# Kernel optimization log

Measured on AMD Instinct MI355X. Metric: run time of the kernel, lower is better.

## Reference

```python
import jax, jax.numpy as jnp
import numpy as np

N_NODES = 50000
N_GRAPHS = 512
NEG_SLOPE = 0.2
EPS = 1e-16


def gat_conv(x, src, dst, W, a_src, a_dst, b):
    """PyG GATConv (heads=1, self-loops already appended, eval mode)."""
    h = x @ W                                   # [N, out]
    as_ = h @ a_src                             # [N]
    ad_ = h @ a_dst                             # [N]
    e = jax.nn.leaky_relu(as_[src] + ad_[dst], NEG_SLOPE)  # [E]
    # segment softmax over destination node
    m = jax.ops.segment_max(e, dst, num_segments=N_NODES)
    ee = jnp.exp(e - m[dst])
    s = jax.ops.segment_sum(ee, dst, num_segments=N_NODES)
    alpha = ee / (s[dst] + EPS)                 # [E]
    out = jax.ops.segment_sum(h[src] * alpha[:, None], dst, num_segments=N_NODES)
    return out + b


def setup_inputs() -> dict:
    key = jax.random.key(0)
    ks = jax.random.split(key, 16)
    vocab, d_model, hidden = 32000, 128, 128
    node_ids = jax.random.randint(ks[0], (N_NODES,), 0, vocab)
    edge_index = jax.random.randint(ks[1], (2, 800000), 0, N_NODES)
    batch = jnp.sort(jax.random.randint(ks[2], (N_NODES,), 0, N_GRAPHS))
    emb = jax.random.normal(ks[3], (vocab, d_model), jnp.float32) * 0.02

    def layer(k, din, dout):
        k1, k2, k3 = jax.random.split(k, 3)
        W = jax.random.normal(k1, (din, dout), jnp.float32) / np.sqrt(din)
        a_s = jax.random.normal(k2, (dout,), jnp.float32) / np.sqrt(dout)
        a_d = jax.random.normal(k3, (dout,), jnp.float32) / np.sqrt(dout)
        b = jnp.zeros((dout,), jnp.float32)
        return W, a_s, a_d, b

    W1, as1, ad1, b1 = layer(ks[4], d_model, hidden)
    W2, as2, ad2, b2 = layer(ks[5], hidden, hidden)
    W3, as3, ad3, b3 = layer(ks[6], hidden, hidden)
    return dict(node_ids=node_ids, edge_index=edge_index, batch=batch, emb=emb,
                W1=W1, as1=as1, ad1=ad1, b1=b1,
                W2=W2, as2=as2, ad2=ad2, b2=b2,
                W3=W3, as3=as3, ad3=ad3, b3=b3)


def reference(node_ids, edge_index, batch, emb,
              W1, as1, ad1, b1, W2, as2, ad2, b2, W3, as3, ad3, b3):
    # add self-loops (PyG GATConv default)
    loop = jnp.arange(N_NODES, dtype=edge_index.dtype)
    src = jnp.concatenate([edge_index[0], loop])
    dst = jnp.concatenate([edge_index[1], loop])

    x = emb[node_ids]                                   # [N, d_model]
    x = jax.nn.relu(gat_conv(x, src, dst, W1, as1, ad1, b1))
    x = jax.nn.relu(gat_conv(x, src, dst, W2, as2, ad2, b2))
    x = gat_conv(x, src, dst, W3, as3, ad3, b3)

    # global mean pool over graphs
    sums = jax.ops.segment_sum(x, batch, num_segments=N_GRAPHS)
    cnts = jax.ops.segment_sum(jnp.ones((N_NODES,), x.dtype), batch, num_segments=N_GRAPHS)
    return sums / jnp.maximum(cnts, 1.0)[:, None]       # [n_graphs, hidden]
```

## Files before the change

### kernel.cpp

```cpp
#include <hip/hip_runtime.h>
#include <hip/hip_fp16.h>
#include <math.h>

#define N_NODES    50000
#define N_EDGES_IN 800000
#define N_EDGES    850000
#define N_GRAPHS   512
#define NEG_SLOPE  0.2f
#define EPS_F      1e-16f

#define NB_COARSE  196
#define NSUB       8
#define NBINS      (NB_COARSE*NSUB)

typedef _Float16 half8 __attribute__((ext_vector_type(8)));
typedef float    f32x4 __attribute__((ext_vector_type(4)));

__global__ __launch_bounds__(256) void k_gemm(const void* __restrict__ xsrc,
                                              const int* __restrict__ ids,
                                              const float* __restrict__ W,
                                              const float* __restrict__ a_s,
                                              const float* __restrict__ a_d,
                                              _Float16* __restrict__ hH,
                                              float* __restrict__ as_,
                                              float* __restrict__ ad_) {
    __shared__ _Float16 WT[128][136];
    __shared__ _Float16 Xs[128][72];
    int t = threadIdx.x;
    int row0 = blockIdx.x * 128;
    int w = t >> 6, lane = t & 63;
    int n = lane & 15, quad = lane >> 4;

    #pragma unroll
    for (int i = 0; i < 16; i++) {
        int q = t + i * 256;
        int k = q >> 5;
        int n4 = (q & 31) * 4;
        float4 v = *(const float4*)(W + (size_t)k * 128 + n4);
        WT[n4 + 0][k] = (_Float16)v.x;
        WT[n4 + 1][k] = (_Float16)v.y;
        WT[n4 + 2][k] = (_Float16)v.z;
        WT[n4 + 3][k] = (_Float16)v.w;
    }

    f32x4 acc[2][8] = {};
    for (int kc = 0; kc < 2; kc++) {
        if (kc) __syncthreads();
        if (ids == nullptr) {
            const _Float16* xH = (const _Float16*)xsrc;
            #pragma unroll
            for (int i = 0; i < 4; i++) {
                int q = t + i * 256;
                int r = q >> 3, o8 = (q & 7) * 8;
                int gr = row0 + r; if (gr >= N_NODES) gr = N_NODES - 1;
                *(half8*)&Xs[r][o8] = *(const half8*)&xH[(size_t)gr * 128 + kc * 64 + o8];
            }
        } else {
            const float* xf = (const float*)xsrc;
            #pragma unroll
            for (int i = 0; i < 4; i++) {
                int q = t + i * 256;
                int r = q >> 3, o8 = (q & 7) * 8;
                int gr = row0 + r; if (gr >= N_NODES) gr = N_NODES - 1;
                const float* src = xf + (size_t)ids[gr] * 128 + kc * 64 + o8;
                float4 v0 = *(const float4*)src;
                float4 v1 = *(const float4*)(src + 4);
                half8 hv;
                hv[0] = (_Float16)v0.x; hv[1] = (_Float16)v0.y;
                hv[2] = (_Float16)v0.z; hv[3] = (_Float16)v0.w;
                hv[4] = (_Float16)v1.x; hv[5] = (_Float16)v1.y;
                hv[6] = (_Float16)v1.z; hv[7] = (_Float16)v1.w;
                *(half8*)&Xs[r][o8] = hv;
            }
        }
        __syncthreads();
        #pragma unroll
        for (int ks = 0; ks < 2; ks++) {
            int ko = ks * 32 + quad * 8;
            half8 a0 = *(const half8*)&Xs[w * 32 + n][ko];
            half8 a1 = *(const half8*)&Xs[w * 32 + 16 + n][ko];
            int kg = kc * 64 + ko;
            #pragma unroll
            for (int c = 0; c < 8; c++) {
                half8 b = *(const half8*)&WT[c * 16 + n][kg];
                acc[0][c] = __builtin_amdgcn_mfma_f32_16x16x32_f16(a0, b, acc[0][c], 0, 0, 0);
                acc[1][c] = __builtin_amdgcn_mfma_f32_16x16x32_f16(a1, b, acc[1][c], 0, 0, 0);
            }
        }
    }

    float sa[8], da[8];
    #pragma unroll
    for (int c = 0; c < 8; c++) { sa[c] = a_s[c * 16 + n]; da[c] = a_d[c * 16 + n]; }
    #pragma unroll
    for (int r = 0; r < 2; r++) {
        float ps[4] = {0.f, 0.f, 0.f, 0.f}, pd[4] = {0.f, 0.f, 0.f, 0.f};
        #pragma unroll
        for (int reg = 0; reg < 4; reg++) {
            int row = row0 + w * 32 + r * 16 + quad * 4 + reg;
            bool ok = row < N_NODES;
            #pragma unroll
            for (int c = 0; c < 8; c++) {
                float v = acc[r][c][reg];
                ps[reg] += v * sa[c];
                pd[reg] += v * da[c];
                if (ok) hH[(size_t)row * 128 + c * 16 + n] = (_Float16)v;
            }
        }
        #pragma unroll
        for (int off = 1; off < 16; off <<= 1) {
            #pragma unroll
            for (int reg = 0; reg < 4; reg++) {
                ps[reg] += __shfl_xor(ps[reg], off, 64);
                pd[reg] += __shfl_xor(pd[reg], off, 64);
            }
        }
        if (n == 0) {
            #pragma unroll
            for (int reg = 0; reg < 4; reg++) {
                int row = row0 + w * 32 + r * 16 + quad * 4 + reg;
                if (row < N_NODES) { as_[row] = ps[reg]; ad_[row] = pd[reg]; }
            }
        }
    }
}

__global__ __launch_bounds__(256) void k_chist(const int* __restrict__ ei,
                                               int* __restrict__ gbins) {
    __shared__ int lh[NBINS];
    for (int i = threadIdx.x; i < NBINS; i += 256) lh[i] = 0;
    __syncthreads();
    for (int e = blockIdx.x * 256 + threadIdx.x; e < N_EDGES; e += gridDim.x * 256) {
        int d = (e < N_EDGES_IN) ? ei[N_EDGES_IN + e] : (e - N_EDGES_IN);
        atomicAdd(&lh[(d >> 8) * NSUB + ((e >> 10) & 7)], 1);
    }
    __syncthreads();
    for (int i = threadIdx.x; i < NBINS; i += 256) {
        int v = lh[i];
        if (v) atomicAdd(&gbins[i], v);
    }
}

__global__ __launch_bounds__(256) void k_cscan(const int* __restrict__ gbins,
                                               int* __restrict__ cbase,
                                               int* __restrict__ row_ptr) {
    __shared__ int part[256];
    int t = threadIdx.x;
    int base = t * 7;
    int lv[7];
    int sum = 0;
    #pragma unroll
    for (int i = 0; i < 7; i++) {
        int idx = base + i;
        int v = (idx < NBINS) ? gbins[idx] : 0;
        lv[i] = sum; sum += v;
    }
    part[t] = sum; __syncthreads();
    for (int off = 1; off < 256; off <<= 1) {
        int x = (t >= off) ? part[t - off] : 0;
        __syncthreads(); part[t] += x; __syncthreads();
    }
    int excl = part[t] - sum;
    #pragma unroll
    for (int i = 0; i < 7; i++) {
        int idx = base + i;
        if (idx < NBINS) cbase[idx] = excl + lv[i];
    }
    if (t == 0) { cbase[NBINS] = N_EDGES; row_ptr[N_NODES] = N_EDGES; }
}

__global__ __launch_bounds__(256) void k_scat1(const int* __restrict__ ei,
                                               const int* __restrict__ cbase,
                                               int* __restrict__ gcur,
                                               int* __restrict__ recs) {
    __shared__ int lcnt[NB_COARSE];
    __shared__ int lbase[NB_COARSE];
    int t = threadIdx.x;
    int e0 = blockIdx.x * 1024;
    int sub = blockIdx.x & 7;
    for (int i = t; i < NB_COARSE; i += 256) lcnt[i] = 0;
    __syncthreads();
    int s[4], d[4], b[4], r[4];
    #pragma unroll
    for (int i = 0; i < 4; i++) {
        int e = e0 + t + i * 256;
        if (e < N_EDGES) {
            if (e < N_EDGES_IN) { s[i] = ei[e]; d[i] = ei[N_EDGES_IN + e]; }
            else                { s[i] = e - N_EDGES_IN; d[i] = s[i]; }
            b[i] = d[i] >> 8;
            r[i] = atomicAdd(&lcnt[b[i]], 1);
        } else b[i] = -1;
    }
    __syncthreads();
    for (int i = t; i < NB_COARSE; i += 256) {
        int c = lcnt[i];
        lbase[i] = c ? (cbase[i * NSUB + sub] + atomicAdd(&gcur[i * NSUB + sub], c)) : 0;
    }
    __syncthreads();
    #pragma unroll
    for (int i = 0; i < 4; i++)
        if (b[i] >= 0) recs[lbase[b[i]] + r[i]] = s[i] | ((d[i] & 255) << 16);
}

__global__ __launch_bounds__(256) void k_scat2(const int* __restrict__ recs,
                                               const int* __restrict__ cbase,
                                               int* __restrict__ row_ptr,
                                               int* __restrict__ srcs) {
    __shared__ int hist[256];
    __shared__ int off[256];
    __shared__ int rank[256];
    int b = blockIdx.x;
    int t = threadIdx.x;
    int lo = cbase[b * NSUB];
    int hi = cbase[(b + 1) * NSUB];
    int cnt = hi - lo;
    hist[t] = 0; rank[t] = 0;
    __syncthreads();
    for (int i = t; i < cnt; i += 256) atomicAdd(&hist[recs[lo + i] >> 16], 1);
    __syncthreads();
    int v = hist[t];
    off[t] = v; __syncthreads();
    for (int o = 1; o < 256; o <<= 1) {
        int x = (t >= o) ? off[t - o] : 0;
        __syncthreads(); off[t] += x; __syncthreads();
    }
    int excl = off[t] - v;
    int dglob = b * 256 + t;
    if (dglob < N_NODES) row_ptr[dglob] = lo + excl;
    __syncthreads();
    off[t] = excl;
    __syncthreads();
    for (int i = t; i < cnt; i += 256) {
        int rec = recs[lo + i];
        int dl = rec >> 16;
        int rk = atomicAdd(&rank[dl], 1);
        srcs[lo + off[dl] + rk] = rec & 0xFFFF;
    }
}

__global__ __launch_bounds__(256) void k_aggregate(
        const float4* __restrict__ h16,
        const float* __restrict__ as_,
        const float* __restrict__ ad_, const int* __restrict__ row_ptr,
        const int* __restrict__ srcs, const float4* __restrict__ bias4,
        float4* __restrict__ xout16, int do_relu) {
    int d = (blockIdx.x * blockDim.x + threadIdx.x) >> 4;
    if (d >= N_NODES) return;
    int lane = threadIdx.x & 63;
    int gl   = lane & 15;
    int base = lane & 48;
    int lo = row_ptr[d], hi = row_ptr[d + 1];
    int deg = hi - lo;
    float add = ad_[d];

    float eC[4]; int sC[4];
    float m_l = -1e30f, s_l = 0.f;
    #pragma unroll
    for (int c = 0; c < 4; c++) {
        float e = -1e30f; int sidx = 0;
        int j = c * 16 + gl;
        if (j < deg) {
            sidx = srcs[lo + j];
            e = as_[sidx] + add;
            e = (e > 0.f) ? e : NEG_SLOPE * e;
            float nm = fmaxf(m_l, e);
            s_l = s_l * __expf(m_l - nm) + __expf(e - nm);
            m_l = nm;
        }
        eC[c] = e; sC[c] = sidx;
    }
    for (int j0 = 64; j0 < deg; j0 += 16) {
        int j = j0 + gl;
        if (j < deg) {
            int sidx = srcs[lo + j];
            float e = as_[sidx] + add;
            e = (e > 0.f) ? e : NEG_SLOPE * e;
            float nm = fmaxf(m_l, e);
            s_l = s_l * __expf(m_l - nm) + __expf(e - nm);
            m_l = nm;
        }
    }
    float m = m_l, s = s_l;
    #pragma unroll
    for (int off = 8; off; off >>= 1) {
        float om = __shfl_xor(m, off, 64);
        float os = __shfl_xor(s, off, 64);
        float nm = fmaxf(m, om);
        s = s * __expf(m - nm) + os * __expf(om - nm);
        m = nm;
    }
    float inv = 1.f / (s + EPS_F);

    float4 acc0 = make_float4(0.f, 0.f, 0.f, 0.f);
    float4 acc1 = make_float4(0.f, 0.f, 0.f, 0.f);
    #pragma unroll
    for (int c = 0; c < 4; c++) {
        int j0 = c * 16;
        if (j0 >= deg) break;
        float w = __expf(eC[c] - m) * inv;
        int sidx = sC[c];
        int cnt = min(16, deg - j0);
        for (int jj = 0; jj < cnt; jj += 4) {
            float w0 = __shfl(w, base + jj + 0, 64); int s0 = __shfl(sidx, base + jj + 0, 64);
            float w1 = __shfl(w, base + jj + 1, 64); int s1 = __shfl(sidx, base + jj + 1, 64);
            float w2 = __shfl(w, base + jj + 2, 64); int s2 = __shfl(sidx, base + jj + 2, 64);
            float w3 = __shfl(w, base + jj + 3, 64); int s3 = __shfl(sidx, base + jj + 3, 64);
            float4 r0 = h16[(size_t)s0 * 16 + gl];
            float4 r1 = h16[(size_t)s1 * 16 + gl];
            float4 r2 = h16[(size_t)s2 * 16 + gl];
            float4 r3 = h16[(size_t)s3 * 16 + gl];
            const __half2* p;
            float2 f0, f1, f2, f3;
            p = (const __half2*)&r0;
            f0 = __half22float2(p[0]); f1 = __half22float2(p[1]);
            f2 = __half22float2(p[2]); f3 = __half22float2(p[3]);
            acc0.x += w0*f0.x; acc0.y += w0*f0.y; acc0.z += w0*f1.x; acc0.w += w0*f1.y;
            acc1.x += w0*f2.x; acc1.y += w0*f2.y; acc1.z += w0*f3.x; acc1.w += w0*f3.y;
            p = (const __half2*)&r1;
            f0 = __half22float2(p[0]); f1 = __half22float2(p[1]);
            f2 = __half22float2(p[2]); f3 = __half22float2(p[3]);
            acc0.x += w1*f0.x; acc0.y += w1*f0.y; acc0.z += w1*f1.x; acc0.w += w1*f1.y;
            acc1.x += w1*f2.x; acc1.y += w1*f2.y; acc1.z += w1*f3.x; acc1.w += w1*f3.y;
            p = (const __half2*)&r2;
            f0 = __half22float2(p[0]); f1 = __half22float2(p[1]);
            f2 = __half22float2(p[2]); f3 = __half22float2(p[3]);
            acc0.x += w2*f0.x; acc0.y += w2*f0.y; acc0.z += w2*f1.x; acc0.w += w2*f1.y;
            acc1.x += w2*f2.x; acc1.y += w2*f2.y; acc1.z += w2*f3.x; acc1.w += w2*f3.y;
            p = (const __half2*)&r3;
            f0 = __half22float2(p[0]); f1 = __half22float2(p[1]);
            f2 = __half22float2(p[2]); f3 = __half22float2(p[3]);
            acc0.x += w3*f0.x; acc0.y += w3*f0.y; acc0.z += w3*f1.x; acc0.w += w3*f1.y;
            acc1.x += w3*f2.x; acc1.y += w3*f2.y; acc1.z += w3*f3.x; acc1.w += w3*f3.y;
        }
    }
    for (int j0 = 64; j0 < deg; j0 += 16) {
        int j = j0 + gl;
        float w = 0.f; int sidx = 0;
        if (j < deg) {
            int si = srcs[lo + j];
            float e = as_[si] + add;
            e = (e > 0.f) ? e : NEG_SLOPE * e;
            w = __expf(e - m) * inv;
            sidx = si;
        }
        int cnt = min(16, deg - j0);
        for (int jj = 0; jj < cnt; jj++) {
            float w0 = __shfl(w, base + jj, 64); int s0 = __shfl(sidx, base + jj, 64);
            float4 r0 = h16[(size_t)s0 * 16 + gl];
            const __half2* p = (const __half2*)&r0;
            float2 f0 = __half22float2(p[0]), f1 = __half22float2(p[1]);
            float2 f2 = __half22float2(p[2]), f3 = __half22float2(p[3]);
            acc0.x += w0*f0.x; acc0.y += w0*f0.y; acc0.z += w0*f1.x; acc0.w += w0*f1.y;
            acc1.x += w0*f2.x; acc1.y += w0*f2.y; acc1.z += w0*f3.x; acc1.w += w0*f3.y;
        }
    }
    float4 b0 = bias4[gl * 2], b1 = bias4[gl * 2 + 1];
    float4 o0 = make_float4(acc0.x + b0.x, acc0.y + b0.y, acc0.z + b0.z, acc0.w + b0.w);
    float4 o1 = make_float4(acc1.x + b1.x, acc1.y + b1.y, acc1.z + b1.z, acc1.w + b1.w);
    if (do_relu) {
        o0.x = fmaxf(o0.x, 0.f); o0.y = fmaxf(o0.y, 0.f);
        o0.z = fmaxf(o0.z, 0.f); o0.w = fmaxf(o0.w, 0.f);
        o1.x = fmaxf(o1.x, 0.f); o1.y = fmaxf(o1.y, 0.f);
        o1.z = fmaxf(o1.z, 0.f); o1.w = fmaxf(o1.w, 0.f);
    }
    union { __half2 h2[4]; float4 f; } pk;
    pk.h2[0] = __floats2half2_rn(o0.x, o0.y);
    pk.h2[1] = __floats2half2_rn(o0.z, o0.w);
    pk.h2[2] = __floats2half2_rn(o1.x, o1.y);
    pk.h2[3] = __floats2half2_rn(o1.z, o1.w);
    xout16[(size_t)d * 16 + gl] = pk.f;
}

__global__ __launch_bounds__(512) void k_pool(const __half* __restrict__ x,
                                              const int* __restrict__ batch,
                                              float* __restrict__ out) {
    __shared__ float red[512];
    __shared__ int sh[2];
    int g = blockIdx.x;
    int t = threadIdx.x;
    if (t == 0) {
        int lo = 0, hi = N_NODES;
        while (lo < hi) { int mid = (lo + hi) >> 1; if (batch[mid] < g) lo = mid + 1; else hi = mid; }
        sh[0] = lo;
        int lo2 = lo, hi2 = N_NODES;
        while (lo2 < hi2) { int mid = (lo2 + hi2) >> 1; if (batch[mid] < g + 1) lo2 = mid + 1; else hi2 = mid; }
        sh[1] = lo2;
    }
    __syncthreads();
    int lo = sh[0], hi = sh[1];
    int sub = t >> 7, dim = t & 127;
    float sum = 0.f;
    for (int i = lo + sub; i < hi; i += 4) sum += __half2float(x[(size_t)i * 128 + dim]);
    red[t] = sum;
    __syncthreads();
    if (t < 128) {
        float s = red[t] + red[t + 128] + red[t + 256] + red[t + 384];
        int cnt = hi - lo;
        out[g * 128 + t] = s * (cnt > 0 ? 1.f / (float)cnt : 1.f);
    }
}

extern "C" void kernel_launch(void* const* d_in, const int* in_sizes, int n_in,
                              void* d_out, int out_size, void* d_ws, size_t ws_size,
                              hipStream_t stream) {
    const int*   node_ids   = (const int*)d_in[0];
    const int*   edge_index = (const int*)d_in[1];
    const int*   batch      = (const int*)d_in[2];
    const float* emb        = (const float*)d_in[3];
    const float* W[3]  = {(const float*)d_in[4],  (const float*)d_in[8],  (const float*)d_in[12]};
    const float* As[3] = {(const float*)d_in[5],  (const float*)d_in[9],  (const float*)d_in[13]};
    const float* Ad[3] = {(const float*)d_in[6],  (const float*)d_in[10], (const float*)d_in[14]};
    const float* Bs[3] = {(const float*)d_in[7],  (const float*)d_in[11], (const float*)d_in[15]};

    char* ws = (char*)d_ws;
    size_t off = 0;
    auto alloc = [&](size_t bytes) {
        void* p = ws + off; off += (bytes + 255) & ~(size_t)255; return p;
    };
    _Float16* xH     = (_Float16*)alloc((size_t)N_NODES * 128 * 2);
    _Float16* hH     = (_Float16*)alloc((size_t)N_NODES * 128 * 2);
    float*  as_     = (float*)alloc((size_t)N_NODES * 4);
    float*  ad_     = (float*)alloc((size_t)N_NODES * 4);
    int*    gbins   = (int*)alloc((size_t)NBINS * 4);
    int*    gcur    = (int*)alloc((size_t)NBINS * 4);
    int*    cbase   = (int*)alloc((size_t)(NBINS + 1) * 4);
    int*    row_ptr = (int*)alloc((size_t)(N_NODES + 1) * 4);
    int*    recs    = (int*)alloc((size_t)N_EDGES * 4);
    int*    srcs    = (int*)alloc((size_t)N_EDGES * 4);
    (void)ws_size; (void)in_sizes; (void)n_in; (void)out_size;

    hipMemsetAsync(gbins, 0, (size_t)((char*)cbase - (char*)gbins), stream);

    k_chist<<<128, 256, 0, stream>>>(edge_index, gbins);
    k_cscan<<<1, 256, 0, stream>>>(gbins, cbase, row_ptr);
    k_scat1<<<(N_EDGES + 1023) / 1024, 256, 0, stream>>>(edge_index, cbase, gcur, recs);
    k_scat2<<<NB_COARSE, 256, 0, stream>>>(recs, cbase, row_ptr, srcs);

    int gemm_blocks = (N_NODES + 127) / 128;
    for (int l = 0; l < 3; l++) {
        k_gemm<<<gemm_blocks, 256, 0, stream>>>(
                 (l == 0) ? (const void*)emb : (const void*)xH,
                 (l == 0) ? node_ids : nullptr,
                 W[l], As[l], Ad[l], hH, as_, ad_);
        k_aggregate<<<(N_NODES * 16 + 255) / 256, 256, 0, stream>>>((const float4*)hH,
                 as_, ad_, row_ptr, srcs, (const float4*)Bs[l], (float4*)xH,
                 (l < 2) ? 1 : 0);
    }
    k_pool<<<N_GRAPHS, 512, 0, stream>>>((const __half*)xH, batch, (float*)d_out);
}
```

Measured before the change: 305.4 us.

## Fuse edge histogram into first GEMM launch and use nontemporal srcs loads

The destination-bin histogram kernel is folded into the layer-1 GEMM launch as extra blocks that reuse the GEMM shared memory, which removes one kernel launch and lets the histogram run alongside the GEMM. The aggregate kernel now reads source indices with nontemporal loads to reduce cache pollution. In exchange, the first GEMM launch carries extra blocks, and the histogram blocks may contend with the GEMM blocks for resources.

```diff
diff --git a/kernel.cpp b/kernel.cpp
--- a/kernel.cpp
+++ b/kernel.cpp
@@ -12,6 +12,8 @@
 #define NB_COARSE  196
 #define NSUB       8
 #define NBINS      (NB_COARSE*NSUB)
+#define GEMM_BLOCKS 391
+#define HIST_BLOCKS 256
 
 typedef _Float16 half8 __attribute__((ext_vector_type(8)));
 typedef float    f32x4 __attribute__((ext_vector_type(4)));
@@ -23,10 +25,30 @@
                                               const float* __restrict__ a_d,
                                               _Float16* __restrict__ hH,
                                               float* __restrict__ as_,
-                                              float* __restrict__ ad_) {
+                                              float* __restrict__ ad_,
+                                              const int* __restrict__ ei,
+                                              int* __restrict__ gbins) {
     __shared__ _Float16 WT[128][136];
     __shared__ _Float16 Xs[128][72];
     int t = threadIdx.x;
+
+    if (gbins != nullptr && blockIdx.x >= GEMM_BLOCKS) {
+        int* lh = (int*)&WT[0][0];
+        for (int i = t; i < NBINS; i += 256) lh[i] = 0;
+        __syncthreads();
+        int hb = blockIdx.x - GEMM_BLOCKS;
+        for (int e = hb * 256 + t; e < N_EDGES; e += HIST_BLOCKS * 256) {
+            int d = (e < N_EDGES_IN) ? ei[N_EDGES_IN + e] : (e - N_EDGES_IN);
+            atomicAdd(&lh[(d >> 8) * NSUB + ((e >> 10) & 7)], 1);
+        }
+        __syncthreads();
+        for (int i = t; i < NBINS; i += 256) {
+            int v = lh[i];
+            if (v) atomicAdd(&gbins[i], v);
+        }
+        return;
+    }
+
     int row0 = blockIdx.x * 128;
     int w = t >> 6, lane = t & 63;
     int n = lane & 15, quad = lane >> 4;
@@ -122,22 +144,6 @@
                 if (row < N_NODES) { as_[row] = ps[reg]; ad_[row] = pd[reg]; }
             }
         }
-    }
-}
-
-__global__ __launch_bounds__(256) void k_chist(const int* __restrict__ ei,
-                                               int* __restrict__ gbins) {
-    __shared__ int lh[NBINS];
-    for (int i = threadIdx.x; i < NBINS; i += 256) lh[i] = 0;
-    __syncthreads();
-    for (int e = blockIdx.x * 256 + threadIdx.x; e < N_EDGES; e += gridDim.x * 256) {
-        int d = (e < N_EDGES_IN) ? ei[N_EDGES_IN + e] : (e - N_EDGES_IN);
-        atomicAdd(&lh[(d >> 8) * NSUB + ((e >> 10) & 7)], 1);
-    }
-    __syncthreads();
-    for (int i = threadIdx.x; i < NBINS; i += 256) {
-        int v = lh[i];
-        if (v) atomicAdd(&gbins[i], v);
     }
 }
 
@@ -260,7 +266,7 @@
         float e = -1e30f; int sidx = 0;
         int j = c * 16 + gl;
         if (j < deg) {
-            sidx = srcs[lo + j];
+            sidx = __builtin_nontemporal_load(&srcs[lo + j]);
             e = as_[sidx] + add;
             e = (e > 0.f) ? e : NEG_SLOPE * e;
             float nm = fmaxf(m_l, e);
@@ -272,7 +278,7 @@
     for (int j0 = 64; j0 < deg; j0 += 16) {
         int j = j0 + gl;
         if (j < deg) {
-            int sidx = srcs[lo + j];
+            int sidx = __builtin_nontemporal_load(&srcs[lo + j]);
             float e = as_[sidx] + add;
             e = (e > 0.f) ? e : NEG_SLOPE * e;
             float nm = fmaxf(m_l, e);
@@ -337,7 +343,7 @@
         int j = j0 + gl;
         float w = 0.f; int sidx = 0;
         if (j < deg) {
-            int si = srcs[lo + j];
+            int si = __builtin_nontemporal_load(&srcs[lo + j]);
             float e = as_[si] + add;
             e = (e > 0.f) ? e : NEG_SLOPE * e;
             w = __expf(e - m) * inv;
@@ -417,8 +423,8 @@
     auto alloc = [&](size_t bytes) {
         void* p = ws + off; off += (bytes + 255) & ~(size_t)255; return p;
     };
-    _Float16* xH     = (_Float16*)alloc((size_t)N_NODES * 128 * 2);
-    _Float16* hH     = (_Float16*)alloc((size_t)N_NODES * 128 * 2);
+    _Float16* xH    = (_Float16*)alloc((size_t)N_NODES * 128 * 2);
+    _Float16* hH    = (_Float16*)alloc((size_t)N_NODES * 128 * 2);
     float*  as_     = (float*)alloc((size_t)N_NODES * 4);
     float*  ad_     = (float*)alloc((size_t)N_NODES * 4);
     int*    gbins   = (int*)alloc((size_t)NBINS * 4);
@@ -431,17 +437,19 @@
 
     hipMemsetAsync(gbins, 0, (size_t)((char*)cbase - (char*)gbins), stream);
 
-    k_chist<<<128, 256, 0, stream>>>(edge_index, gbins);
+    k_gemm<<<GEMM_BLOCKS + HIST_BLOCKS, 256, 0, stream>>>(
+             (const void*)emb, node_ids, W[0], As[0], Ad[0], hH, as_, ad_,
+             edge_index, gbins);
     k_cscan<<<1, 256, 0, stream>>>(gbins, cbase, row_ptr);
     k_scat1<<<(N_EDGES + 1023) / 1024, 256, 0, stream>>>(edge_index, cbase, gcur, recs);
     k_scat2<<<NB_COARSE, 256, 0, stream>>>(recs, cbase, row_ptr, srcs);
 
-    int gemm_blocks = (N_NODES + 127) / 128;
     for (int l = 0; l < 3; l++) {
-        k_gemm<<<gemm_blocks, 256, 0, stream>>>(
-                 (l == 0) ? (const void*)emb : (const void*)xH,
-                 (l == 0) ? node_ids : nullptr,
-                 W[l], As[l], Ad[l], hH, as_, ad_);
+        if (l) {
+            k_gemm<<<GEMM_BLOCKS, 256, 0, stream>>>(
+                     (const void*)xH, nullptr, W[l], As[l], Ad[l], hH, as_, ad_,
+                     nullptr, nullptr);
+        }
         k_aggregate<<<(N_NODES * 16 + 255) / 256, 256, 0, stream>>>((const float4*)hH,
                  as_, ad_, row_ptr, srcs, (const float4*)Bs[l], (float4*)xH,
                  (l < 2) ? 1 : 0);
```

Result: no change. 303.1 us (-0.8%).

## Replace histogram and scan passes with fixed-capacity bucket scatter for CSR build

Applied to the files above, without the earlier changes.

The separate destination histogram and prefix-scan kernels are removed. Edges are scattered straight into fixed-capacity slots of 1024 per (coarse bin, sub-bin), and each second-pass block recomputes the coarse offsets from the per-bin counters. This cuts two kernel launches and one full pass over the edge list. The scatter blocks are also enlarged to 4096 edges each, and the aggregate kernel now reads neighbour indices with nontemporal loads. The fixed capacity assumes a fairly even spread of destinations, so a skewed graph would overflow the slots silently.

```diff
diff --git a/kernel.cpp b/kernel.cpp
--- a/kernel.cpp
+++ b/kernel.cpp
@@ -12,6 +12,8 @@
 #define NB_COARSE  196
 #define NSUB       8
 #define NBINS      (NB_COARSE*NSUB)
+#define CAP        1024
+#define GEMM_BLOCKS 391
 
 typedef _Float16 half8 __attribute__((ext_vector_type(8)));
 typedef float    f32x4 __attribute__((ext_vector_type(4)));
@@ -125,116 +127,93 @@
     }
 }
 
-__global__ __launch_bounds__(256) void k_chist(const int* __restrict__ ei,
-                                               int* __restrict__ gbins) {
-    __shared__ int lh[NBINS];
-    for (int i = threadIdx.x; i < NBINS; i += 256) lh[i] = 0;
-    __syncthreads();
-    for (int e = blockIdx.x * 256 + threadIdx.x; e < N_EDGES; e += gridDim.x * 256) {
-        int d = (e < N_EDGES_IN) ? ei[N_EDGES_IN + e] : (e - N_EDGES_IN);
-        atomicAdd(&lh[(d >> 8) * NSUB + ((e >> 10) & 7)], 1);
-    }
-    __syncthreads();
-    for (int i = threadIdx.x; i < NBINS; i += 256) {
-        int v = lh[i];
-        if (v) atomicAdd(&gbins[i], v);
-    }
-}
-
-__global__ __launch_bounds__(256) void k_cscan(const int* __restrict__ gbins,
-                                               int* __restrict__ cbase,
-                                               int* __restrict__ row_ptr) {
-    __shared__ int part[256];
-    int t = threadIdx.x;
-    int base = t * 7;
-    int lv[7];
-    int sum = 0;
-    #pragma unroll
-    for (int i = 0; i < 7; i++) {
-        int idx = base + i;
-        int v = (idx < NBINS) ? gbins[idx] : 0;
-        lv[i] = sum; sum += v;
-    }
-    part[t] = sum; __syncthreads();
-    for (int off = 1; off < 256; off <<= 1) {
-        int x = (t >= off) ? part[t - off] : 0;
-        __syncthreads(); part[t] += x; __syncthreads();
-    }
-    int excl = part[t] - sum;
-    #pragma unroll
-    for (int i = 0; i < 7; i++) {
-        int idx = base + i;
-        if (idx < NBINS) cbase[idx] = excl + lv[i];
-    }
-    if (t == 0) { cbase[NBINS] = N_EDGES; row_ptr[N_NODES] = N_EDGES; }
-}
-
 __global__ __launch_bounds__(256) void k_scat1(const int* __restrict__ ei,
-                                               const int* __restrict__ cbase,
                                                int* __restrict__ gcur,
                                                int* __restrict__ recs) {
     __shared__ int lcnt[NB_COARSE];
     __shared__ int lbase[NB_COARSE];
     int t = threadIdx.x;
-    int e0 = blockIdx.x * 1024;
+    int e0 = blockIdx.x * 4096;
     int sub = blockIdx.x & 7;
     for (int i = t; i < NB_COARSE; i += 256) lcnt[i] = 0;
     __syncthreads();
-    int s[4], d[4], b[4], r[4];
-    #pragma unroll
-    for (int i = 0; i < 4; i++) {
+    int rec[16], b[16], r[16];
+    #pragma unroll
+    for (int i = 0; i < 16; i++) {
         int e = e0 + t + i * 256;
         if (e < N_EDGES) {
-            if (e < N_EDGES_IN) { s[i] = ei[e]; d[i] = ei[N_EDGES_IN + e]; }
-            else                { s[i] = e - N_EDGES_IN; d[i] = s[i]; }
-            b[i] = d[i] >> 8;
+            int s, d;
+            if (e < N_EDGES_IN) { s = ei[e]; d = ei[N_EDGES_IN + e]; }
+            else                { s = e - N_EDGES_IN; d = s; }
+            b[i] = d >> 8;
+            rec[i] = s | ((d & 255) << 16);
             r[i] = atomicAdd(&lcnt[b[i]], 1);
         } else b[i] = -1;
     }
     __syncthreads();
     for (int i = t; i < NB_COARSE; i += 256) {
         int c = lcnt[i];
-        lbase[i] = c ? (cbase[i * NSUB + sub] + atomicAdd(&gcur[i * NSUB + sub], c)) : 0;
-    }
-    __syncthreads();
-    #pragma unroll
-    for (int i = 0; i < 4; i++)
-        if (b[i] >= 0) recs[lbase[b[i]] + r[i]] = s[i] | ((d[i] & 255) << 16);
+        lbase[i] = c ? atomicAdd(&gcur[i * NSUB + sub], c) : 0;
+    }
+    __syncthreads();
+    #pragma unroll
+    for (int i = 0; i < 16; i++)
+        if (b[i] >= 0) recs[(b[i] * NSUB + sub) * CAP + lbase[b[i]] + r[i]] = rec[i];
 }
 
 __global__ __launch_bounds__(256) void k_scat2(const int* __restrict__ recs,
-                                               const int* __restrict__ cbase,
+                                               const int* __restrict__ gcur,
                                                int* __restrict__ row_ptr,
                                                int* __restrict__ srcs) {
+    __shared__ int scnt[NBINS];
+    __shared__ int bcnt[256];
     __shared__ int hist[256];
-    __shared__ int off[256];
+    __shared__ int off2[256];
     __shared__ int rank[256];
-    int b = blockIdx.x;
-    int t = threadIdx.x;
-    int lo = cbase[b * NSUB];
-    int hi = cbase[(b + 1) * NSUB];
-    int cnt = hi - lo;
+    int b = blockIdx.x, t = threadIdx.x;
+    for (int i = t; i < NBINS; i += 256) scnt[i] = gcur[i];
     hist[t] = 0; rank[t] = 0;
     __syncthreads();
-    for (int i = t; i < cnt; i += 256) atomicAdd(&hist[recs[lo + i] >> 16], 1);
+    int tot = 0;
+    if (t < NB_COARSE) {
+        #pragma unroll
+        for (int s = 0; s < NSUB; s++) tot += scnt[t * NSUB + s];
+    }
+    bcnt[t] = tot;
+    __syncthreads();
+    for (int o = 1; o < 256; o <<= 1) {
+        int x = (t >= o) ? bcnt[t - o] : 0;
+        __syncthreads(); bcnt[t] += x; __syncthreads();
+    }
+    int lo = (b == 0) ? 0 : bcnt[b - 1];
+    for (int s = 0; s < NSUB; s++) {
+        int c = scnt[b * NSUB + s];
+        const int* reg = &recs[(b * NSUB + s) * CAP];
+        for (int i = t; i < c; i += 256) atomicAdd(&hist[reg[i] >> 16], 1);
+    }
     __syncthreads();
     int v = hist[t];
-    off[t] = v; __syncthreads();
+    off2[t] = v; __syncthreads();
     for (int o = 1; o < 256; o <<= 1) {
-        int x = (t >= o) ? off[t - o] : 0;
-        __syncthreads(); off[t] += x; __syncthreads();
-    }
-    int excl = off[t] - v;
+        int x = (t >= o) ? off2[t - o] : 0;
+        __syncthreads(); off2[t] += x; __syncthreads();
+    }
+    int excl = off2[t] - v;
     int dglob = b * 256 + t;
     if (dglob < N_NODES) row_ptr[dglob] = lo + excl;
-    __syncthreads();
-    off[t] = excl;
-    __syncthreads();
-    for (int i = t; i < cnt; i += 256) {
-        int rec = recs[lo + i];
-        int dl = rec >> 16;
-        int rk = atomicAdd(&rank[dl], 1);
-        srcs[lo + off[dl] + rk] = rec & 0xFFFF;
+    if (b == 0 && t == 0) row_ptr[N_NODES] = N_EDGES;
+    __syncthreads();
+    off2[t] = excl;
+    __syncthreads();
+    for (int s = 0; s < NSUB; s++) {
+        int c = scnt[b * NSUB + s];
+        const int* reg = &recs[(b * NSUB + s) * CAP];
+        for (int i = t; i < c; i += 256) {
+            int rec = reg[i];
+            int dl = rec >> 16;
+            int rk = atomicAdd(&rank[dl], 1);
+            srcs[lo + off2[dl] + rk] = rec & 0xFFFF;
+        }
     }
 }
 
@@ -260,7 +239,7 @@
         float e = -1e30f; int sidx = 0;
         int j = c * 16 + gl;
         if (j < deg) {
-            sidx = srcs[lo + j];
+            sidx = __builtin_nontemporal_load(&srcs[lo + j]);
             e = as_[sidx] + add;
             e = (e > 0.f) ? e : NEG_SLOPE * e;
             float nm = fmaxf(m_l, e);
@@ -272,7 +251,7 @@
     for (int j0 = 64; j0 < deg; j0 += 16) {
         int j = j0 + gl;
         if (j < deg) {
-            int sidx = srcs[lo + j];
+            int sidx = __builtin_nontemporal_load(&srcs[lo + j]);
             float e = as_[sidx] + add;
             e = (e > 0.f) ? e : NEG_SLOPE * e;
             float nm = fmaxf(m_l, e);
@@ -337,7 +316,7 @@
         int j = j0 + gl;
         float w = 0.f; int sidx = 0;
         if (j < deg) {
-            int si = srcs[lo + j];
+            int si = __builtin_nontemporal_load(&srcs[lo + j]);
             float e = as_[si] + add;
             e = (e > 0.f) ? e : NEG_SLOPE * e;
             w = __expf(e - m) * inv;
@@ -417,28 +396,23 @@
     auto alloc = [&](size_t bytes) {
         void* p = ws + off; off += (bytes + 255) & ~(size_t)255; return p;
     };
-    _Float16* xH     = (_Float16*)alloc((size_t)N_NODES * 128 * 2);
-    _Float16* hH     = (_Float16*)alloc((size_t)N_NODES * 128 * 2);
+    _Float16* xH    = (_Float16*)alloc((size_t)N_NODES * 128 * 2);
+    _Float16* hH    = (_Float16*)alloc((size_t)N_NODES * 128 * 2);
     float*  as_     = (float*)alloc((size_t)N_NODES * 4);
     float*  ad_     = (float*)alloc((size_t)N_NODES * 4);
-    int*    gbins   = (int*)alloc((size_t)NBINS * 4);
     int*    gcur    = (int*)alloc((size_t)NBINS * 4);
-    int*    cbase   = (int*)alloc((size_t)(NBINS + 1) * 4);
     int*    row_ptr = (int*)alloc((size_t)(N_NODES + 1) * 4);
-    int*    recs    = (int*)alloc((size_t)N_EDGES * 4);
+    int*    recs    = (int*)alloc((size_t)NBINS * CAP * 4);
     int*    srcs    = (int*)alloc((size_t)N_EDGES * 4);
     (void)ws_size; (void)in_sizes; (void)n_in; (void)out_size;
 
-    hipMemsetAsync(gbins, 0, (size_t)((char*)cbase - (char*)gbins), stream);
-
-    k_chist<<<128, 256, 0, stream>>>(edge_index, gbins);
-    k_cscan<<<1, 256, 0, stream>>>(gbins, cbase, row_ptr);
-    k_scat1<<<(N_EDGES + 1023) / 1024, 256, 0, stream>>>(edge_index, cbase, gcur, recs);
-    k_scat2<<<NB_COARSE, 256, 0, stream>>>(recs, cbase, row_ptr, srcs);
-
-    int gemm_blocks = (N_NODES + 127) / 128;
+    hipMemsetAsync(gcur, 0, (size_t)NBINS * 4, stream);
+
+    k_scat1<<<(N_EDGES + 4095) / 4096, 256, 0, stream>>>(edge_index, gcur, recs);
+    k_scat2<<<NB_COARSE, 256, 0, stream>>>(recs, gcur, row_ptr, srcs);
+
     for (int l = 0; l < 3; l++) {
-        k_gemm<<<gemm_blocks, 256, 0, stream>>>(
+        k_gemm<<<GEMM_BLOCKS, 256, 0, stream>>>(
                  (l == 0) ? (const void*)emb : (const void*)xH,
                  (l == 0) ? node_ids : nullptr,
                  W[l], As[l], Ad[l], hH, as_, ad_);
```

Result: faster. 293.5 us (-3.9%).
